# Performance work log

Measured on AMD Instinct MI355X. Metric: run time of the kernel, lower is better.

The kernel has to match this reference:

```python
import jax, jax.numpy as jnp
import numpy as np

NUM_CLASSES = 5  # fill_max for graph_label


def setup_inputs() -> dict:
    key = jax.random.key(0)
    k1, k2, k3, k4, k5, k6 = jax.random.split(key, 6)
    z_dim, hid = 64, 256  # hid = 4 * z_dim
    G, N = 16, 40000      # set_length, set_size
    graph_input = jax.random.normal(k1, (G, N, z_dim), dtype=jnp.float32)
    graph_label = jax.random.randint(k2, (N,), 0, NUM_CLASSES)
    # GraphConvolution params, uniform(-stdv, stdv) with stdv = 1/sqrt(out_features)
    s1 = 1.0 / np.sqrt(hid)
    s2 = 1.0 / np.sqrt(z_dim)
    W1 = jax.random.uniform(k3, (z_dim, hid), minval=-s1, maxval=s1, dtype=jnp.float32)
    b1 = jax.random.uniform(k4, (hid,), minval=-s1, maxval=s1, dtype=jnp.float32)
    W2 = jax.random.uniform(k5, (hid, z_dim), minval=-s2, maxval=s2, dtype=jnp.float32)
    b2 = jax.random.uniform(k6, (z_dim,), minval=-s2, maxval=s2, dtype=jnp.float32)
    return {"graph_input": graph_input, "graph_label": graph_label,
            "W1": W1, "b1": b1, "W2": W2, "b2": b2}


def reference(graph_input, graph_label, W1, b1, W2, b2):
    # The label-induced adjacency (same-class clique + self loop, row-normalized)
    # has rows equal to 1/n_c over the node's class, so spmm(adj, x) is the
    # per-class mean of x. Dropout is identity in eval mode.
    dt = graph_input.dtype
    onehot = (graph_label[None, :] == jnp.arange(NUM_CLASSES)[:, None]).astype(dt)  # [C,N]
    counts = jnp.maximum(onehot.sum(axis=1), jnp.asarray(1, dt))                    # [C]

    def gcn(x, W, b):
        support = jnp.einsum('gnd,df->gnf', x, W)                              # dense mm
        cls_mean = jnp.einsum('cn,gnf->gcf', onehot, support) / counts[None, :, None]
        return cls_mean[:, graph_label, :] + b                                 # spmm + bias

    h = jax.nn.relu(gcn(graph_input, W1, b1))
    return graph_input + gcn(h, W2, b2)
```

## Files before the change

### kernel.cpp

```cpp
#include <hip/hip_runtime.h>

#define G 16
#define N 40000
#define D 64
#define HID 256
#define C 5
#define CHUNK 400
#define NCHUNK (N / CHUNK)

typedef float v4f __attribute__((ext_vector_type(4)));


__global__ __launch_bounds__(256) void k_sums(const v4f* __restrict__ x,
                                              const int* __restrict__ lab,
                                              float* __restrict__ S,
                                              float* __restrict__ cntf) {
    const int g    = blockIdx.y;
    const int base = blockIdx.x * CHUNK;
    const int tid  = threadIdx.x;
    const int q    = tid & 15;
    const int r    = tid >> 4;

    v4f acc[C];
    float cacc[C];
#pragma unroll
    for (int c = 0; c < C; ++c) { acc[c] = (v4f)0.f; cacc[c] = 0.f; }

    const v4f* xg = x + (size_t)g * N * 16;
    for (int i = r; i < CHUNK; i += 16) {
        const int n   = base + i;
        const int lbl = lab[n];
        v4f v = xg[(size_t)n * 16 + q];
#pragma unroll
        for (int c = 0; c < C; ++c) {
            const float m = (lbl == c) ? 1.f : 0.f;
            acc[c] += m * v;
            cacc[c] += m;
        }
    }

    __shared__ v4f   red[C][16][16];
    __shared__ float scnt[C][16];
#pragma unroll
    for (int c = 0; c < C; ++c) {
        red[c][r][q] = acc[c];
        if (q == 0) scnt[c][r] = cacc[c];
    }
    __syncthreads();
    for (int s = 8; s >= 1; s >>= 1) {
        if (r < s) {
#pragma unroll
            for (int c = 0; c < C; ++c) {
                red[c][r][q] += red[c][r + s][q];
                if (q == 0) scnt[c][r] += scnt[c][r + s];
            }
        }
        __syncthreads();
    }
    if (r == 0) {
#pragma unroll
        for (int c = 0; c < C; ++c) {
            v4f a = red[c][0][q];
            float* dst = S + ((g * C + c) * D) + q * 4;
            atomicAdd(dst + 0, a.x);
            atomicAdd(dst + 1, a.y);
            atomicAdd(dst + 2, a.z);
            atomicAdd(dst + 3, a.w);
            if (q == 0 && g == 0) atomicAdd(&cntf[c], scnt[c][0]);
        }
    }
}

__global__ __launch_bounds__(256) void k_mlp(const float* __restrict__ S,
                                             const float* __restrict__ cntf,
                                             const float* __restrict__ W1,
                                             const float* __restrict__ b1,
                                             const float* __restrict__ W2,
                                             const float* __restrict__ b2,
                                             float* __restrict__ M2) {
    const int gc  = blockIdx.x;
    const int tid = threadIdx.x;
    __shared__ float xm[D];
    __shared__ float H[HID];
    if (tid < D) {
        float cc = cntf[gc % C];
        if (cc < 1.f) cc = 1.f;
        xm[tid] = S[gc * D + tid] / cc;
    }
    __syncthreads();
    float m1 = 0.f;
#pragma unroll
    for (int d = 0; d < D; ++d) m1 = fmaf(xm[d], W1[d * HID + tid], m1);
    m1 += b1[tid];
    H[tid] = m1 > 0.f ? m1 : 0.f;
    __syncthreads();
    if (tid < D) {
        float m2 = 0.f;
        for (int f = 0; f < HID; ++f) m2 = fmaf(H[f], W2[f * D + tid], m2);
        M2[gc * D + tid] = m2 + b2[tid];
    }
}

__global__ __launch_bounds__(256) void k_out(const v4f* __restrict__ x,
                                             const int* __restrict__ lab,
                                             const v4f* __restrict__ M2,
                                             v4f* __restrict__ out) {
    const int g    = blockIdx.y;
    const int base = blockIdx.x * CHUNK;
    const int tid  = threadIdx.x;
    const int q    = tid & 15;
    const int r    = tid >> 4;

    __shared__ v4f m2s[C][16];
    if (tid < C * 16) m2s[tid >> 4][tid & 15] = M2[(size_t)g * C * 16 + tid];
    __syncthreads();

    const size_t goff = (size_t)g * N * 16;
    for (int i = r; i < CHUNK; i += 16) {
        const int n   = base + i;
        const int lbl = lab[n];
        v4f v = x[goff + (size_t)n * 16 + q];
        v += m2s[lbl][q];
        __builtin_nontemporal_store(v, out + goff + (size_t)n * 16 + q);
    }
}

extern "C" void kernel_launch(void* const* d_in, const int* in_sizes, int n_in,
                              void* d_out, int out_size, void* d_ws, size_t ws_size,
                              hipStream_t stream) {
    const float* x   = (const float*)d_in[0];
    const int*   lab = (const int*)d_in[1];
    const float* W1  = (const float*)d_in[2];
    const float* b1  = (const float*)d_in[3];
    const float* W2  = (const float*)d_in[4];
    const float* b2  = (const float*)d_in[5];
    float* out = (float*)d_out;

    char*  ws   = (char*)d_ws;
    float* S    = (float*)ws;
    float* cntf = (float*)(ws + 20480);
    float* M2   = (float*)(ws + 20736);

    hipMemsetAsync(d_ws, 0, 20512, stream);

    dim3 grid(NCHUNK, G);
    k_sums<<<grid, 256, 0, stream>>>((const v4f*)x, lab, S, cntf);

    k_mlp<<<G * C, 256, 0, stream>>>(S, cntf, W1, b1, W2, b2, M2);

    k_out<<<grid, 256, 0, stream>>>((const v4f*)x, lab, (const v4f*)M2,
                                    (v4f*)out);
}
```

Measured before the change: 331.4 us.

## Replace atomic class-sum reduction with per-block partials reduced in MLP kernel

The sums kernel now writes per-block partial class sums and counts to a workspace buffer instead of issuing global atomicAdds. It uses fewer, larger chunks (50 blocks of 800 nodes per graph), and the MLP kernel reduces the partials before the dense layers. This removes the memset and the contention from float atomics, at the cost of an extra partial buffer and a small reduction step in the MLP kernel. The streaming loops also get unroll-by-2 pragmas.

```diff
diff --git a/kernel.cpp b/kernel.cpp
--- a/kernel.cpp
+++ b/kernel.cpp
@@ -5,18 +5,23 @@
 #define D 64
 #define HID 256
 #define C 5
-#define CHUNK 400
-#define NCHUNK (N / CHUNK)
+
+#define NB 50
+#define CHUNKS 800
+
+#define CHUNKO 400
+#define NBO (N / CHUNKO)
 
 typedef float v4f __attribute__((ext_vector_type(4)));
 
 
 __global__ __launch_bounds__(256) void k_sums(const v4f* __restrict__ x,
                                               const int* __restrict__ lab,
-                                              float* __restrict__ S,
-                                              float* __restrict__ cntf) {
+                                              v4f* __restrict__ Spart,
+                                              float* __restrict__ cntpart) {
     const int g    = blockIdx.y;
-    const int base = blockIdx.x * CHUNK;
+    const int b    = blockIdx.x;
+    const int base = b * CHUNKS;
     const int tid  = threadIdx.x;
     const int q    = tid & 15;
     const int r    = tid >> 4;
@@ -27,7 +32,8 @@
     for (int c = 0; c < C; ++c) { acc[c] = (v4f)0.f; cacc[c] = 0.f; }
 
     const v4f* xg = x + (size_t)g * N * 16;
-    for (int i = r; i < CHUNK; i += 16) {
+#pragma unroll 2
+    for (int i = r; i < CHUNKS; i += 16) {
         const int n   = base + i;
         const int lbl = lab[n];
         v4f v = xg[(size_t)n * 16 + q];
@@ -59,38 +65,52 @@
     }
     if (r == 0) {
 #pragma unroll
-        for (int c = 0; c < C; ++c) {
-            v4f a = red[c][0][q];
-            float* dst = S + ((g * C + c) * D) + q * 4;
-            atomicAdd(dst + 0, a.x);
-            atomicAdd(dst + 1, a.y);
-            atomicAdd(dst + 2, a.z);
-            atomicAdd(dst + 3, a.w);
-            if (q == 0 && g == 0) atomicAdd(&cntf[c], scnt[c][0]);
-        }
+        for (int c = 0; c < C; ++c)
+            Spart[(((size_t)g * NB + b) * C + c) * 16 + q] = red[c][0][q];
     }
+    if (g == 0 && tid < C)
+        cntpart[b * C + tid] = scnt[tid][0];
 }
 
-__global__ __launch_bounds__(256) void k_mlp(const float* __restrict__ S,
-                                             const float* __restrict__ cntf,
+__global__ __launch_bounds__(256) void k_mlp(const float* __restrict__ Spart,
+                                             const float* __restrict__ cntpart,
                                              const float* __restrict__ W1,
                                              const float* __restrict__ b1,
                                              const float* __restrict__ W2,
                                              const float* __restrict__ b2,
                                              float* __restrict__ M2) {
     const int gc  = blockIdx.x;
+    const int g   = gc / C;
+    const int c   = gc % C;
     const int tid = threadIdx.x;
+    const int d   = tid & 63;
+    const int grp = tid >> 6;
+
+    __shared__ float rs[4][D];
+    __shared__ float ccnt;
     __shared__ float xm[D];
     __shared__ float H[HID];
+
+    float s = 0.f;
+    for (int b = grp; b < NB; b += 4)
+        s += Spart[(((size_t)g * NB + b) * C + c) * D + d];
+    rs[grp][d] = s;
+
+    if (tid == 0) ccnt = 0.f;
+    __syncthreads();
+    if (tid < NB) atomicAdd(&ccnt, cntpart[tid * C + c]);
+    __syncthreads();
+
     if (tid < D) {
-        float cc = cntf[gc % C];
+        float cc = ccnt;
         if (cc < 1.f) cc = 1.f;
-        xm[tid] = S[gc * D + tid] / cc;
+        xm[tid] = (rs[0][tid] + rs[1][tid] + rs[2][tid] + rs[3][tid]) / cc;
     }
     __syncthreads();
+
     float m1 = 0.f;
 #pragma unroll
-    for (int d = 0; d < D; ++d) m1 = fmaf(xm[d], W1[d * HID + tid], m1);
+    for (int dd = 0; dd < D; ++dd) m1 = fmaf(xm[dd], W1[dd * HID + tid], m1);
     m1 += b1[tid];
     H[tid] = m1 > 0.f ? m1 : 0.f;
     __syncthreads();
@@ -106,7 +126,7 @@
                                              const v4f* __restrict__ M2,
                                              v4f* __restrict__ out) {
     const int g    = blockIdx.y;
-    const int base = blockIdx.x * CHUNK;
+    const int base = blockIdx.x * CHUNKO;
     const int tid  = threadIdx.x;
     const int q    = tid & 15;
     const int r    = tid >> 4;
@@ -116,7 +136,8 @@
     __syncthreads();
 
     const size_t goff = (size_t)g * N * 16;
-    for (int i = r; i < CHUNK; i += 16) {
+#pragma unroll 2
+    for (int i = r; i < CHUNKO; i += 16) {
         const int n   = base + i;
         const int lbl = lab[n];
         v4f v = x[goff + (size_t)n * 16 + q];
@@ -136,18 +157,17 @@
     const float* b2  = (const float*)d_in[5];
     float* out = (float*)d_out;
 
-    char*  ws   = (char*)d_ws;
-    float* S    = (float*)ws;
-    float* cntf = (float*)(ws + 20480);
-    float* M2   = (float*)(ws + 20736);
+    float* wsf     = (float*)d_ws;
+    float* Spart   = wsf;
+    float* cntpart = wsf + 256000;
+    float* M2      = wsf + 256256;
 
-    hipMemsetAsync(d_ws, 0, 20512, stream);
+    dim3 gs(NB, G);
+    k_sums<<<gs, 256, 0, stream>>>((const v4f*)x, lab, (v4f*)Spart, cntpart);
 
-    dim3 grid(NCHUNK, G);
-    k_sums<<<grid, 256, 0, stream>>>((const v4f*)x, lab, S, cntf);
+    k_mlp<<<G * C, 256, 0, stream>>>(Spart, cntpart, W1, b1, W2, b2, M2);
 
-    k_mlp<<<G * C, 256, 0, stream>>>(S, cntf, W1, b1, W2, b2, M2);
-
-    k_out<<<grid, 256, 0, stream>>>((const v4f*)x, lab, (const v4f*)M2,
-                                    (v4f*)out);
+    dim3 go(NBO, G);
+    k_out<<<go, 256, 0, stream>>>((const v4f*)x, lab, (const v4f*)M2,
+                                  (v4f*)out);
 }
```

New measurement: 329.1 us. About the same (-0.7%).
